# Optimization experiments

Measured on AMD Instinct MI355X. Metric: run time of the kernel, lower is better.

Reference implementation:

```python
import jax, jax.numpy as jnp
import numpy as np
from jax import lax

B, L, D_IN, H, RES, BD, D_OUT = 1024, 128, 5, 64, 256, 8, 1


def setup_inputs() -> dict:
    key = jax.random.key(0)
    ks = jax.random.split(key, 14)
    f = jnp.float32
    d = {}
    d["V_noise"] = jax.random.normal(ks[0], (B, D_IN), f)
    d["increments"] = jax.random.normal(ks[1], (B, L, BD), f)
    d["W1"] = jax.random.normal(ks[2], (H, D_IN), f) / np.float32(np.sqrt(D_IN))
    d["b1"] = jnp.zeros((H,), f)
    d["W2"] = jax.random.normal(ks[3], (RES, H), f) / np.float32(np.sqrt(H))
    d["b2"] = jnp.zeros((RES,), f)
    d["rho1"] = jax.random.normal(ks[4], (1, 1), f)
    d["rho2"] = jax.random.normal(ks[5], (1, 1), f)
    d["rho3"] = jax.random.normal(ks[6], (1, 1), f)
    d["rho4"] = jax.random.normal(ks[7], (1, 1), f)
    d["rho5"] = jax.random.normal(ks[8], (1, 1), f)
    # scale reservoir matrices by 1/sqrt(res) so pre-activations are O(1)
    d["B1"] = jax.random.normal(ks[9], (RES, RES), f) / np.float32(np.sqrt(RES))
    d["B2"] = jax.random.normal(ks[10], (BD, RES, RES), f) / np.float32(np.sqrt(RES))
    d["lambda1"] = jax.random.normal(ks[11], (RES, 1), f)
    d["lambda2"] = jax.random.normal(ks[12], (BD, RES, 1), f)
    d["Wr"] = jax.random.normal(ks[13], (D_OUT, RES), f) / np.float32(np.sqrt(RES))
    d["br"] = jnp.zeros((D_OUT,), f)
    return d


def reference(V_noise, increments, W1, b1, W2, b2,
              rho1, rho2, rho3, rho4, rho5,
              B1, B2, lambda1, lambda2, Wr, br):
    act = jnp.tanh
    # initial-condition MLP: [B, D_in] -> [B, RES]
    V = act(V_noise @ W1.T + b1) @ W2.T + b2
    # Brownian path with W[:,0] = 0
    Wp = jnp.cumsum(increments, axis=1).at[:, 0, :].set(0.0)
    dW = Wp[:, 1:] - Wp[:, :-1]          # [B, L-1, BD]
    l1 = lambda1[:, 0]                    # [RES]
    l2 = lambda2[:, :, 0]                 # [BD, RES]
    rho5s = rho5[0, 0]

    def step(r, dw):                      # r: [B, RES], dw: [B, BD]
        drift = act(rho1 * (r @ B1.T) + rho2 * l1)                      # [B, RES]
        diff = act(rho3 * jnp.einsum('kij,bj->bki', B2, r) + rho4 * l2)  # [B, BD, RES]
        rn = r + drift + rho5s * jnp.einsum('bki,bk->bi', diff, dw)
        return rn, rn

    _, Rs = lax.scan(step, V, jnp.swapaxes(dW, 0, 1))  # [L-1, B, RES]
    Rall = jnp.concatenate([V[None], Rs], axis=0)       # [L, B, RES]
    # time-homogeneous linear readout per lag, concatenated along time
    x = Rall @ Wr.T + br                                 # [L, B, D_out]
    out = jnp.transpose(x, (1, 0, 2)).reshape(V.shape[0], Rall.shape[0] * x.shape[-1], 1)
    return out
```

## Files before the change

### kernel.cpp

```cpp
#include <hip/hip_runtime.h>
#include <hip/hip_bf16.h>

#define B_TOT 1024
#define L_T   128
#define DIN   5
#define HD    64
#define RESN  256
#define BDN   8
#define NMAT  9
#define NROWS (NMAT * RESN)
#define PLANE ((size_t)NROWS * RESN)
#define NGRP  16
#define BG    64
#define FPB   16
#define NTHR  256
#define RB_GRP (2 * BG * RESN)
#define WS_RB_OFF  (2 * PLANE * 2)
#define WS_FLAG_OFF (WS_RB_OFF + (size_t)NGRP * RB_GRP * 4)
#define FLAGS_PER_GRP 1024

typedef __attribute__((ext_vector_type(8))) short bf16x8;
typedef __attribute__((ext_vector_type(4))) float f32x4;

__device__ __forceinline__ float fast_tanh(float x) {
    float e = __expf(2.0f * x);
    return 1.0f - 2.0f * __builtin_amdgcn_rcpf(e + 1.0f);
}

__device__ __forceinline__ unsigned pack_hilo(float v) {
    __hip_bfloat16 hi = __float2bfloat16(v);
    __hip_bfloat16 lo = __float2bfloat16(v - __bfloat162float(hi));
    return (unsigned)__builtin_bit_cast(unsigned short, hi) |
           ((unsigned)__builtin_bit_cast(unsigned short, lo) << 16);
}

__device__ __forceinline__ uint4 mall_load4(const unsigned* p) {
    uint4 r;
    asm volatile("global_load_dwordx4 %0, %1, off sc0 sc1" : "=v"(r) : "v"(p));
    return r;
}
__device__ __forceinline__ unsigned mall_load1(const unsigned* p) {
    unsigned r;
    asm volatile("global_load_dword %0, %1, off sc0 sc1" : "=v"(r) : "v"(p));
    return r;
}
__device__ __forceinline__ void mall_store1(unsigned* p, unsigned v) {
    asm volatile("global_store_dword %0, %1, off sc0 sc1" :: "v"(p), "v"(v) : "memory");
}
__device__ __forceinline__ void wait_vm0() {
    asm volatile("s_waitcnt vmcnt(0)" ::: "memory");
}

__device__ __forceinline__ void spin_all(const unsigned* fladdr, unsigned want) {
    unsigned guard = 0;
    for (;;) {
        unsigned fv = mall_load1(fladdr);
        wait_vm0();
        if (__ballot(fv < want) == 0ull) break;
        __builtin_amdgcn_s_sleep(1);
        if (++guard > (1u << 20)) break;
    }
}

__global__ void conv_w(const float* __restrict__ B1, const float* __restrict__ B2,
                       __hip_bfloat16* __restrict__ wh, __hip_bfloat16* __restrict__ wl) {
    int idx = blockIdx.x * 256 + threadIdx.x;
    float v = (idx < RESN * RESN) ? B1[idx] : B2[idx - RESN * RESN];
    __hip_bfloat16 h = __float2bfloat16(v);
    wh[idx] = h;
    wl[idx] = __float2bfloat16(v - __bfloat162float(h));
}

__global__ __launch_bounds__(NTHR, 1) void sde_ws(
    const float* __restrict__ Vn,  const float* __restrict__ inc,
    const float* __restrict__ W1,  const float* __restrict__ b1,
    const float* __restrict__ W2,  const float* __restrict__ b2,
    const float* __restrict__ rho1p, const float* __restrict__ rho2p,
    const float* __restrict__ rho3p, const float* __restrict__ rho4p,
    const float* __restrict__ rho5p,
    const float* __restrict__ lam1, const float* __restrict__ lam2,
    const float* __restrict__ Wr,  const float* __restrict__ brp,
    const __hip_bfloat16* __restrict__ wbf,
    unsigned int* __restrict__ rbu,
    unsigned int* __restrict__ flags,
    float* __restrict__ out)
{
    __shared__ __align__(16) short wlds[2][NMAT][8][64][8];
    __shared__ __align__(16) short wrlds[2][8][4][8];
    __shared__ __align__(16) short zfrag[8];

    const int tid  = threadIdx.x;
    const int mt   = tid >> 6;
    const int lane = tid & 63;
    const int n16  = lane & 15;
    const int quad = lane >> 4;
    const int bx   = blockIdx.x;
    const int g    = ((bx & 7) << 1) | (bx >> 7);
    const int fb   = (bx >> 3) & 15;
    const int f0   = fb * FPB;
    const int b0g  = g * BG;
    unsigned int* rbg    = rbu + (size_t)g * RB_GRP;
    unsigned int* flagp  = flags + g * FLAGS_PER_GRP;
    unsigned int* myflag = flagp + (fb * 4 + mt) * 16;
    const unsigned* fladdr = (const unsigned*)(flagp + ((lane & 15) * 4 + mt) * 16);

    const float rho1 = rho1p[0], rho2 = rho2p[0], rho3 = rho3p[0],
                rho4 = rho4p[0], rho5 = rho5p[0];
    const float brv = brp[0];

    float* hf  = (float*)&wlds[0][0][0][0][0];
    float* vsh = hf + 64 * 66;
    for (int p = tid; p < BG * HD; p += NTHR) {
        int b = p >> 6, hh = p & 63;
        float s = b1[hh];
        #pragma unroll
        for (int d = 0; d < DIN; ++d) s += Vn[(b0g + b) * DIN + d] * W1[hh * DIN + d];
        hf[b * 66 + hh] = fast_tanh(s);
    }
    __syncthreads();
    {
        int b = 16 * mt + (lane >> 2);
        #pragma unroll
        for (int i = 0; i < 4; ++i) {
            int f = (lane & 3) * 4 + i;
            float s = b2[f0 + f];
            #pragma unroll 8
            for (int hh = 0; hh < HD; ++hh) s += hf[b * 66 + hh] * W2[(f0 + f) * HD + hh];
            vsh[b * 16 + f] = s;
            mall_store1(&rbg[(0 * BG + b) * RESN + f0 + f], pack_hilo(s));
        }
    }
    wait_vm0();
    if (lane == 0)
        __hip_atomic_fetch_add(myflag, 1u, __ATOMIC_RELAXED, __HIP_MEMORY_SCOPE_AGENT);

    float rmast[4];
    #pragma unroll
    for (int rg = 0; rg < 4; ++rg) rmast[rg] = vsh[(16 * mt + 4 * quad + rg) * 16 + n16];
    const float l1c = lam1[f0 + n16];
    float l2c[BDN];
    #pragma unroll
    for (int k = 0; k < BDN; ++k) l2c[k] = lam2[k * RESN + f0 + n16];
    __syncthreads();

    for (int e = tid; e < 2 * NMAT * 8 * 64; e += NTHR) {
        int l  = e & 63;
        int kk = (e >> 6) & 7;
        int m  = e >> 9;
        int pl = (m >= NMAT) ? 1 : 0;
        int nt = m - pl * NMAT;
        const uint4* src = (const uint4*)(wbf + (size_t)pl * PLANE +
            (size_t)(nt * RESN + f0 + (l & 15)) * RESN + kk * 32 + (l >> 4) * 8);
        *(uint4*)&wlds[pl][nt][kk][l][0] = *src;
    }
    for (int p = tid; p < 512; p += NTHR) {
        int s = p >> 3, j = p & 7;
        int pl = s >> 5, kk = (s >> 2) & 7, q = s & 3;
        float v = Wr[kk * 32 + q * 8 + j];
        __hip_bfloat16 hi = __float2bfloat16(v);
        wrlds[pl][kk][q][j] = pl ? __builtin_bit_cast(short, __float2bfloat16(v - __bfloat162float(hi)))
                                 : __builtin_bit_cast(short, hi);
    }
    if (tid < 8) zfrag[tid] = 0;
    __syncthreads();

    const short* ph = (n16 == 0) ? &wrlds[0][0][quad][0] : &zfrag[0];
    const short* pw = (n16 == 0) ? &wrlds[1][0][quad][0] : &zfrag[0];
    const int    stp = (n16 == 0) ? 4 * 8 : 0;

    for (int t = 0; t < L_T - 1; ++t) {
        float dwv[4][8];
        #pragma unroll
        for (int rg = 0; rg < 4; ++rg) {
            const size_t bglob = (size_t)(b0g + 16 * mt + 4 * quad + rg) * (L_T * BDN);
            const float4 d0 = *(const float4*)(inc + bglob + (size_t)(t + 1) * BDN);
            const float4 d1 = *(const float4*)(inc + bglob + (size_t)(t + 1) * BDN + 4);
            dwv[rg][0] = d0.x; dwv[rg][1] = d0.y; dwv[rg][2] = d0.z; dwv[rg][3] = d0.w;
            dwv[rg][4] = d1.x; dwv[rg][5] = d1.y; dwv[rg][6] = d1.z; dwv[rg][7] = d1.w;
            if (t == 0) {
                const float4 e0 = *(const float4*)(inc + bglob);
                const float4 e1 = *(const float4*)(inc + bglob + 4);
                dwv[rg][0] += e0.x; dwv[rg][1] += e0.y; dwv[rg][2] += e0.z; dwv[rg][3] += e0.w;
                dwv[rg][4] += e1.x; dwv[rg][5] += e1.y; dwv[rg][6] += e1.z; dwv[rg][7] += e1.w;
            }
        }
        spin_all(fladdr, (unsigned)(t + 1));
        const int cur = t & 1, nxt = cur ^ 1;
        const int lead = t & 15;

        uint4 ua[16];
        {
            const unsigned* rbc = rbg + (size_t)(cur * BG + 16 * mt + n16) * RESN + quad * 8;
            #pragma unroll
            for (int kk = 0; kk < 8; ++kk) {
                ua[2 * kk]     = mall_load4(rbc + kk * 32);
                ua[2 * kk + 1] = mall_load4(rbc + kk * 32 + 4);
            }
        }
        wait_vm0();
        bf16x8 afh[8], afl[8];
        #pragma unroll
        for (int kk = 0; kk < 8; ++kk) {
            const uint4 a = ua[2 * kk], b = ua[2 * kk + 1];
            unsigned hw[4], lw[4];
            hw[0] = __builtin_amdgcn_perm(a.y, a.x, 0x05040100u);
            hw[1] = __builtin_amdgcn_perm(a.w, a.z, 0x05040100u);
            hw[2] = __builtin_amdgcn_perm(b.y, b.x, 0x05040100u);
            hw[3] = __builtin_amdgcn_perm(b.w, b.z, 0x05040100u);
            lw[0] = __builtin_amdgcn_perm(a.y, a.x, 0x07060302u);
            lw[1] = __builtin_amdgcn_perm(a.w, a.z, 0x07060302u);
            lw[2] = __builtin_amdgcn_perm(b.y, b.x, 0x07060302u);
            lw[3] = __builtin_amdgcn_perm(b.w, b.z, 0x07060302u);
            afh[kk] = __builtin_bit_cast(bf16x8, *(__attribute__((ext_vector_type(4))) unsigned*)hw);
            afl[kk] = __builtin_bit_cast(bf16x8, *(__attribute__((ext_vector_type(4))) unsigned*)lw);
        }

        f32x4 acc[NMAT] = {};
        #pragma unroll
        for (int kk = 0; kk < 8; ++kk) {
            bf16x8 bh[NMAT], bl[NMAT];
            #pragma unroll
            for (int nt = 0; nt < NMAT; ++nt) {
                bh[nt] = *(const bf16x8*)&wlds[0][nt][kk][lane][0];
                bl[nt] = *(const bf16x8*)&wlds[1][nt][kk][lane][0];
            }
            #pragma unroll
            for (int nt = 0; nt < NMAT; ++nt)
                acc[nt] = __builtin_amdgcn_mfma_f32_16x16x32_bf16(afh[kk], bh[nt], acc[nt], 0, 0, 0);
            #pragma unroll
            for (int nt = 0; nt < NMAT; ++nt)
                acc[nt] = __builtin_amdgcn_mfma_f32_16x16x32_bf16(afl[kk], bh[nt], acc[nt], 0, 0, 0);
            #pragma unroll
            for (int nt = 0; nt < NMAT; ++nt)
                acc[nt] = __builtin_amdgcn_mfma_f32_16x16x32_bf16(afh[kk], bl[nt], acc[nt], 0, 0, 0);
        }

        #pragma unroll
        for (int rg = 0; rg < 4; ++rg) {
            const int bl_ = 16 * mt + 4 * quad + rg;
            float drift = fast_tanh(rho1 * acc[0][rg] + rho2 * l1c);
            float s = 0.0f;
            #pragma unroll
            for (int k = 0; k < BDN; ++k)
                s += fast_tanh(rho3 * acc[1 + k][rg] + rho4 * l2c[k]) * dwv[rg][k];
            float rn = rmast[rg] + drift + rho5 * s;
            rmast[rg] = rn;
            mall_store1(&rbg[(nxt * BG + bl_) * RESN + f0 + n16], pack_hilo(rn));
        }
        wait_vm0();
        if (lane == 0)
            __hip_atomic_fetch_add(myflag, 1u, __ATOMIC_RELAXED, __HIP_MEMORY_SCOPE_AGENT);

        if (fb == lead) {
            f32x4 accw = {};
            #pragma unroll
            for (int kk = 0; kk < 8; ++kk) {
                bf16x8 wh8 = *(const bf16x8*)(ph + kk * stp);
                bf16x8 wl8 = *(const bf16x8*)(pw + kk * stp);
                accw = __builtin_amdgcn_mfma_f32_16x16x32_bf16(afh[kk], wh8, accw, 0, 0, 0);
                accw = __builtin_amdgcn_mfma_f32_16x16x32_bf16(afl[kk], wh8, accw, 0, 0, 0);
                accw = __builtin_amdgcn_mfma_f32_16x16x32_bf16(afh[kk], wl8, accw, 0, 0, 0);
            }
            if (n16 == 0) {
                #pragma unroll
                for (int rg = 0; rg < 4; ++rg)
                    out[(size_t)(b0g + 16 * mt + 4 * quad + rg) * L_T + t] = accw[rg] + brv;
            }
        }
    }

    if (fb == 15) {
        spin_all(fladdr, (unsigned)L_T);
        uint4 ua[16];
        const unsigned* rbc = rbg + (size_t)(1 * BG + 16 * mt + n16) * RESN + quad * 8;
        #pragma unroll
        for (int kk = 0; kk < 8; ++kk) {
            ua[2 * kk]     = mall_load4(rbc + kk * 32);
            ua[2 * kk + 1] = mall_load4(rbc + kk * 32 + 4);
        }
        wait_vm0();
        f32x4 accw = {};
        #pragma unroll
        for (int kk = 0; kk < 8; ++kk) {
            const uint4 a = ua[2 * kk], b = ua[2 * kk + 1];
            unsigned hw[4], lw[4];
            hw[0] = __builtin_amdgcn_perm(a.y, a.x, 0x05040100u);
            hw[1] = __builtin_amdgcn_perm(a.w, a.z, 0x05040100u);
            hw[2] = __builtin_amdgcn_perm(b.y, b.x, 0x05040100u);
            hw[3] = __builtin_amdgcn_perm(b.w, b.z, 0x05040100u);
            lw[0] = __builtin_amdgcn_perm(a.y, a.x, 0x07060302u);
            lw[1] = __builtin_amdgcn_perm(a.w, a.z, 0x07060302u);
            lw[2] = __builtin_amdgcn_perm(b.y, b.x, 0x07060302u);
            lw[3] = __builtin_amdgcn_perm(b.w, b.z, 0x07060302u);
            bf16x8 ah = __builtin_bit_cast(bf16x8, *(__attribute__((ext_vector_type(4))) unsigned*)hw);
            bf16x8 al = __builtin_bit_cast(bf16x8, *(__attribute__((ext_vector_type(4))) unsigned*)lw);
            bf16x8 wh8 = *(const bf16x8*)(ph + kk * stp);
            bf16x8 wl8 = *(const bf16x8*)(pw + kk * stp);
            accw = __builtin_amdgcn_mfma_f32_16x16x32_bf16(ah, wh8, accw, 0, 0, 0);
            accw = __builtin_amdgcn_mfma_f32_16x16x32_bf16(al, wh8, accw, 0, 0, 0);
            accw = __builtin_amdgcn_mfma_f32_16x16x32_bf16(ah, wl8, accw, 0, 0, 0);
        }
        if (n16 == 0) {
            #pragma unroll
            for (int rg = 0; rg < 4; ++rg)
                out[(size_t)(b0g + 16 * mt + 4 * quad + rg) * L_T + (L_T - 1)] = accw[rg] + brv;
        }
    }
}

extern "C" void kernel_launch(void* const* d_in, const int* in_sizes, int n_in,
                              void* d_out, int out_size, void* d_ws, size_t ws_size,
                              hipStream_t stream) {
    const float* Vn   = (const float*)d_in[0];
    const float* inc  = (const float*)d_in[1];
    const float* W1   = (const float*)d_in[2];
    const float* b1   = (const float*)d_in[3];
    const float* W2   = (const float*)d_in[4];
    const float* b2   = (const float*)d_in[5];
    const float* r1   = (const float*)d_in[6];
    const float* r2   = (const float*)d_in[7];
    const float* r3   = (const float*)d_in[8];
    const float* r4   = (const float*)d_in[9];
    const float* r5   = (const float*)d_in[10];
    const float* B1   = (const float*)d_in[11];
    const float* B2   = (const float*)d_in[12];
    const float* lam1 = (const float*)d_in[13];
    const float* lam2 = (const float*)d_in[14];
    const float* Wr   = (const float*)d_in[15];
    const float* br   = (const float*)d_in[16];

    __hip_bfloat16* wh    = (__hip_bfloat16*)d_ws;
    unsigned int*   rbu   = (unsigned int*)((char*)d_ws + WS_RB_OFF);
    unsigned int*   flags = (unsigned int*)((char*)d_ws + WS_FLAG_OFF);
    float* out = (float*)d_out;

    hipMemsetAsync(flags, 0, NGRP * FLAGS_PER_GRP * sizeof(unsigned int), stream);
    conv_w<<<dim3(NROWS * RESN / 256), dim3(256), 0, stream>>>(B1, B2, wh, wh + PLANE);
    sde_ws<<<dim3(256), dim3(NTHR), 0, stream>>>(
        Vn, inc, W1, b1, W2, b2, r1, r2, r3, r4, r5, lam1, lam2, Wr, br,
        wh, rbu, flags, out);
}
```

Measured before the change: 873.1 us.

## Replace flag-based inter-block sync with tagged data words and register-resident weights

The separate flag counters and atomic increments are removed. Each step now embeds a 2-bit step tag in the low bits of the packed hi/lo state words, and consumers spin directly on the state data until every tag matches. This drops one round trip of flag polling plus the store-drain wait per step. It also keeps 3 of the 9 weight matrices in registers and only 6 in LDS, and fuses the readout MFMA into the main k-loop. In exchange, the low bf16 word loses two mantissa bits, which slightly lowers precision, and register pressure rises.

```diff
diff --git a/kernel.cpp b/kernel.cpp
--- a/kernel.cpp
+++ b/kernel.cpp
@@ -8,6 +8,8 @@
 #define RESN  256
 #define BDN   8
 #define NMAT  9
+#define NMAT_REG 3
+#define NMAT_LDS 6
 #define NROWS (NMAT * RESN)
 #define PLANE ((size_t)NROWS * RESN)
 #define NGRP  16
@@ -16,8 +18,6 @@
 #define NTHR  256
 #define RB_GRP (2 * BG * RESN)
 #define WS_RB_OFF  (2 * PLANE * 2)
-#define WS_FLAG_OFF (WS_RB_OFF + (size_t)NGRP * RB_GRP * 4)
-#define FLAGS_PER_GRP 1024
 
 typedef __attribute__((ext_vector_type(8))) short bf16x8;
 typedef __attribute__((ext_vector_type(4))) float f32x4;
@@ -27,11 +27,12 @@
     return 1.0f - 2.0f * __builtin_amdgcn_rcpf(e + 1.0f);
 }
 
-__device__ __forceinline__ unsigned pack_hilo(float v) {
+__device__ __forceinline__ unsigned pack_hilo_tag(float v, unsigned tag16) {
     __hip_bfloat16 hi = __float2bfloat16(v);
     __hip_bfloat16 lo = __float2bfloat16(v - __bfloat162float(hi));
-    return (unsigned)__builtin_bit_cast(unsigned short, hi) |
-           ((unsigned)__builtin_bit_cast(unsigned short, lo) << 16);
+    unsigned pv = (unsigned)__builtin_bit_cast(unsigned short, hi) |
+                  ((unsigned)__builtin_bit_cast(unsigned short, lo) << 16);
+    return (pv & 0xFFFCFFFFu) | tag16;
 }
 
 __device__ __forceinline__ uint4 mall_load4(const unsigned* p) {
@@ -39,11 +40,6 @@
     asm volatile("global_load_dwordx4 %0, %1, off sc0 sc1" : "=v"(r) : "v"(p));
     return r;
 }
-__device__ __forceinline__ unsigned mall_load1(const unsigned* p) {
-    unsigned r;
-    asm volatile("global_load_dword %0, %1, off sc0 sc1" : "=v"(r) : "v"(p));
-    return r;
-}
 __device__ __forceinline__ void mall_store1(unsigned* p, unsigned v) {
     asm volatile("global_store_dword %0, %1, off sc0 sc1" :: "v"(p), "v"(v) : "memory");
 }
@@ -51,15 +47,19 @@
     asm volatile("s_waitcnt vmcnt(0)" ::: "memory");
 }
 
-__device__ __forceinline__ void spin_all(const unsigned* fladdr, unsigned want) {
-    unsigned guard = 0;
-    for (;;) {
-        unsigned fv = mall_load1(fladdr);
-        wait_vm0();
-        if (__ballot(fv < want) == 0ull) break;
-        __builtin_amdgcn_s_sleep(1);
-        if (++guard > (1u << 20)) break;
-    }
+__device__ __forceinline__ void unpack_af(const uint4 a, const uint4 b,
+                                          bf16x8& afh, bf16x8& afl) {
+    unsigned hw[4], lw[4];
+    hw[0] = __builtin_amdgcn_perm(a.y, a.x, 0x05040100u);
+    hw[1] = __builtin_amdgcn_perm(a.w, a.z, 0x05040100u);
+    hw[2] = __builtin_amdgcn_perm(b.y, b.x, 0x05040100u);
+    hw[3] = __builtin_amdgcn_perm(b.w, b.z, 0x05040100u);
+    lw[0] = __builtin_amdgcn_perm(a.y, a.x, 0x07060302u) & 0xFFFCFFFCu;
+    lw[1] = __builtin_amdgcn_perm(a.w, a.z, 0x07060302u) & 0xFFFCFFFCu;
+    lw[2] = __builtin_amdgcn_perm(b.y, b.x, 0x07060302u) & 0xFFFCFFFCu;
+    lw[3] = __builtin_amdgcn_perm(b.w, b.z, 0x07060302u) & 0xFFFCFFFCu;
+    afh = __builtin_bit_cast(bf16x8, *(__attribute__((ext_vector_type(4))) unsigned*)hw);
+    afl = __builtin_bit_cast(bf16x8, *(__attribute__((ext_vector_type(4))) unsigned*)lw);
 }
 
 __global__ void conv_w(const float* __restrict__ B1, const float* __restrict__ B2,
@@ -69,6 +69,12 @@
     __hip_bfloat16 h = __float2bfloat16(v);
     wh[idx] = h;
     wl[idx] = __float2bfloat16(v - __bfloat162float(h));
+}
+
+__global__ void init_rb(unsigned* __restrict__ rbu) {
+    unsigned idx = blockIdx.x * 256 + threadIdx.x;
+    unsigned buf = (idx & (RB_GRP - 1)) >> 14;
+    rbu[idx] = buf ? 0x00000000u : 0x00010000u;
 }
 
 __global__ __launch_bounds__(NTHR, 1) void sde_ws(
@@ -82,10 +88,9 @@
     const float* __restrict__ Wr,  const float* __restrict__ brp,
     const __hip_bfloat16* __restrict__ wbf,
     unsigned int* __restrict__ rbu,
-    unsigned int* __restrict__ flags,
     float* __restrict__ out)
 {
-    __shared__ __align__(16) short wlds[2][NMAT][8][64][8];
+    __shared__ __align__(16) short wlds[2][NMAT_LDS][8][64][8];
     __shared__ __align__(16) short wrlds[2][8][4][8];
     __shared__ __align__(16) short zfrag[8];
 
@@ -99,10 +104,7 @@
     const int fb   = (bx >> 3) & 15;
     const int f0   = fb * FPB;
     const int b0g  = g * BG;
-    unsigned int* rbg    = rbu + (size_t)g * RB_GRP;
-    unsigned int* flagp  = flags + g * FLAGS_PER_GRP;
-    unsigned int* myflag = flagp + (fb * 4 + mt) * 16;
-    const unsigned* fladdr = (const unsigned*)(flagp + ((lane & 15) * 4 + mt) * 16);
+    unsigned int* rbg = rbu + (size_t)g * RB_GRP;
 
     const float rho1 = rho1p[0], rho2 = rho2p[0], rho3 = rho3p[0],
                 rho4 = rho4p[0], rho5 = rho5p[0];
@@ -127,13 +129,9 @@
             #pragma unroll 8
             for (int hh = 0; hh < HD; ++hh) s += hf[b * 66 + hh] * W2[(f0 + f) * HD + hh];
             vsh[b * 16 + f] = s;
-            mall_store1(&rbg[(0 * BG + b) * RESN + f0 + f], pack_hilo(s));
-        }
-    }
-    wait_vm0();
-    if (lane == 0)
-        __hip_atomic_fetch_add(myflag, 1u, __ATOMIC_RELAXED, __HIP_MEMORY_SCOPE_AGENT);
-
+            mall_store1(&rbg[(0 * BG + b) * RESN + f0 + f], pack_hilo_tag(s, 0u));
+        }
+    }
     float rmast[4];
     #pragma unroll
     for (int rg = 0; rg < 4; ++rg) rmast[rg] = vsh[(16 * mt + 4 * quad + rg) * 16 + n16];
@@ -143,14 +141,23 @@
     for (int k = 0; k < BDN; ++k) l2c[k] = lam2[k * RESN + f0 + n16];
     __syncthreads();
 
-    for (int e = tid; e < 2 * NMAT * 8 * 64; e += NTHR) {
+    bf16x8 Brh[NMAT_REG][8], Brl[NMAT_REG][8];
+    #pragma unroll
+    for (int nt = 0; nt < NMAT_REG; ++nt)
+        #pragma unroll
+        for (int kk = 0; kk < 8; ++kk) {
+            const size_t a = (size_t)(nt * RESN + f0 + n16) * RESN + kk * 32 + quad * 8;
+            Brh[nt][kk] = *(const bf16x8*)(wbf + a);
+            Brl[nt][kk] = *(const bf16x8*)(wbf + PLANE + a);
+        }
+    for (int e = tid; e < 2 * NMAT_LDS * 8 * 64; e += NTHR) {
         int l  = e & 63;
         int kk = (e >> 6) & 7;
         int m  = e >> 9;
-        int pl = (m >= NMAT) ? 1 : 0;
-        int nt = m - pl * NMAT;
+        int pl = (m >= NMAT_LDS) ? 1 : 0;
+        int nt = m - pl * NMAT_LDS;
         const uint4* src = (const uint4*)(wbf + (size_t)pl * PLANE +
-            (size_t)(nt * RESN + f0 + (l & 15)) * RESN + kk * 32 + (l >> 4) * 8);
+            (size_t)((NMAT_REG + nt) * RESN + f0 + (l & 15)) * RESN + kk * 32 + (l >> 4) * 8);
         *(uint4*)&wlds[pl][nt][kk][l][0] = *src;
     }
     for (int p = tid; p < 512; p += NTHR) {
@@ -184,57 +191,66 @@
                 dwv[rg][4] += e1.x; dwv[rg][5] += e1.y; dwv[rg][6] += e1.z; dwv[rg][7] += e1.w;
             }
         }
-        spin_all(fladdr, (unsigned)(t + 1));
         const int cur = t & 1, nxt = cur ^ 1;
         const int lead = t & 15;
+        const unsigned exp16 = ((unsigned)(t & 3)) << 16;
+        const unsigned* rbc = rbg + (size_t)(cur * BG + 16 * mt + n16) * RESN + quad * 8;
 
         uint4 ua[16];
         {
-            const unsigned* rbc = rbg + (size_t)(cur * BG + 16 * mt + n16) * RESN + quad * 8;
-            #pragma unroll
-            for (int kk = 0; kk < 8; ++kk) {
-                ua[2 * kk]     = mall_load4(rbc + kk * 32);
-                ua[2 * kk + 1] = mall_load4(rbc + kk * 32 + 4);
-            }
-        }
-        wait_vm0();
-        bf16x8 afh[8], afl[8];
+            unsigned guard = 0;
+            for (;;) {
+                #pragma unroll
+                for (int kk = 0; kk < 8; ++kk) {
+                    ua[2 * kk]     = mall_load4(rbc + kk * 32);
+                    ua[2 * kk + 1] = mall_load4(rbc + kk * 32 + 4);
+                }
+                wait_vm0();
+                unsigned bad = 0;
+                #pragma unroll
+                for (int i = 0; i < 16; ++i)
+                    bad |= (ua[i].x ^ exp16) | (ua[i].y ^ exp16) |
+                           (ua[i].z ^ exp16) | (ua[i].w ^ exp16);
+                bad &= 0x00030000u;
+                if (__ballot(bad != 0) == 0ull) break;
+                __builtin_amdgcn_s_sleep(1);
+                if (++guard > (1u << 20)) break;
+            }
+        }
+
+        f32x4 acc[NMAT] = {};
+        f32x4 accw = {};
         #pragma unroll
         for (int kk = 0; kk < 8; ++kk) {
-            const uint4 a = ua[2 * kk], b = ua[2 * kk + 1];
-            unsigned hw[4], lw[4];
-            hw[0] = __builtin_amdgcn_perm(a.y, a.x, 0x05040100u);
-            hw[1] = __builtin_amdgcn_perm(a.w, a.z, 0x05040100u);
-            hw[2] = __builtin_amdgcn_perm(b.y, b.x, 0x05040100u);
-            hw[3] = __builtin_amdgcn_perm(b.w, b.z, 0x05040100u);
-            lw[0] = __builtin_amdgcn_perm(a.y, a.x, 0x07060302u);
-            lw[1] = __builtin_amdgcn_perm(a.w, a.z, 0x07060302u);
-            lw[2] = __builtin_amdgcn_perm(b.y, b.x, 0x07060302u);
-            lw[3] = __builtin_amdgcn_perm(b.w, b.z, 0x07060302u);
-            afh[kk] = __builtin_bit_cast(bf16x8, *(__attribute__((ext_vector_type(4))) unsigned*)hw);
-            afl[kk] = __builtin_bit_cast(bf16x8, *(__attribute__((ext_vector_type(4))) unsigned*)lw);
-        }
-
-        f32x4 acc[NMAT] = {};
-        #pragma unroll
-        for (int kk = 0; kk < 8; ++kk) {
+            bf16x8 afh, afl;
+            unpack_af(ua[2 * kk], ua[2 * kk + 1], afh, afl);
             bf16x8 bh[NMAT], bl[NMAT];
             #pragma unroll
-            for (int nt = 0; nt < NMAT; ++nt) {
-                bh[nt] = *(const bf16x8*)&wlds[0][nt][kk][lane][0];
-                bl[nt] = *(const bf16x8*)&wlds[1][nt][kk][lane][0];
+            for (int nt = 0; nt < NMAT_REG; ++nt) { bh[nt] = Brh[nt][kk]; bl[nt] = Brl[nt][kk]; }
+            #pragma unroll
+            for (int nt = 0; nt < NMAT_LDS; ++nt) {
+                bh[NMAT_REG + nt] = *(const bf16x8*)&wlds[0][nt][kk][lane][0];
+                bl[NMAT_REG + nt] = *(const bf16x8*)&wlds[1][nt][kk][lane][0];
             }
             #pragma unroll
             for (int nt = 0; nt < NMAT; ++nt)
-                acc[nt] = __builtin_amdgcn_mfma_f32_16x16x32_bf16(afh[kk], bh[nt], acc[nt], 0, 0, 0);
+                acc[nt] = __builtin_amdgcn_mfma_f32_16x16x32_bf16(afh, bh[nt], acc[nt], 0, 0, 0);
             #pragma unroll
             for (int nt = 0; nt < NMAT; ++nt)
-                acc[nt] = __builtin_amdgcn_mfma_f32_16x16x32_bf16(afl[kk], bh[nt], acc[nt], 0, 0, 0);
+                acc[nt] = __builtin_amdgcn_mfma_f32_16x16x32_bf16(afl, bh[nt], acc[nt], 0, 0, 0);
             #pragma unroll
             for (int nt = 0; nt < NMAT; ++nt)
-                acc[nt] = __builtin_amdgcn_mfma_f32_16x16x32_bf16(afh[kk], bl[nt], acc[nt], 0, 0, 0);
-        }
-
+                acc[nt] = __builtin_amdgcn_mfma_f32_16x16x32_bf16(afh, bl[nt], acc[nt], 0, 0, 0);
+            if (fb == lead) {
+                bf16x8 wh8 = *(const bf16x8*)(ph + kk * stp);
+                bf16x8 wl8 = *(const bf16x8*)(pw + kk * stp);
+                accw = __builtin_amdgcn_mfma_f32_16x16x32_bf16(afh, wh8, accw, 0, 0, 0);
+                accw = __builtin_amdgcn_mfma_f32_16x16x32_bf16(afl, wh8, accw, 0, 0, 0);
+                accw = __builtin_amdgcn_mfma_f32_16x16x32_bf16(afh, wl8, accw, 0, 0, 0);
+            }
+        }
+
+        const unsigned tag16 = ((unsigned)((t + 1) & 3)) << 16;
         #pragma unroll
         for (int rg = 0; rg < 4; ++rg) {
             const int bl_ = 16 * mt + 4 * quad + rg;
@@ -245,60 +261,48 @@
                 s += fast_tanh(rho3 * acc[1 + k][rg] + rho4 * l2c[k]) * dwv[rg][k];
             float rn = rmast[rg] + drift + rho5 * s;
             rmast[rg] = rn;
-            mall_store1(&rbg[(nxt * BG + bl_) * RESN + f0 + n16], pack_hilo(rn));
-        }
-        wait_vm0();
-        if (lane == 0)
-            __hip_atomic_fetch_add(myflag, 1u, __ATOMIC_RELAXED, __HIP_MEMORY_SCOPE_AGENT);
-
-        if (fb == lead) {
-            f32x4 accw = {};
+            mall_store1(&rbg[(nxt * BG + bl_) * RESN + f0 + n16], pack_hilo_tag(rn, tag16));
+        }
+
+        if (fb == lead && n16 == 0) {
+            #pragma unroll
+            for (int rg = 0; rg < 4; ++rg)
+                out[(size_t)(b0g + 16 * mt + 4 * quad + rg) * L_T + t] = accw[rg] + brv;
+        }
+    }
+
+    if (fb == 15) {
+        const unsigned exp16 = 3u << 16;
+        const unsigned* rbc = rbg + (size_t)(1 * BG + 16 * mt + n16) * RESN + quad * 8;
+        uint4 ua[16];
+        unsigned guard = 0;
+        for (;;) {
             #pragma unroll
             for (int kk = 0; kk < 8; ++kk) {
-                bf16x8 wh8 = *(const bf16x8*)(ph + kk * stp);
-                bf16x8 wl8 = *(const bf16x8*)(pw + kk * stp);
-                accw = __builtin_amdgcn_mfma_f32_16x16x32_bf16(afh[kk], wh8, accw, 0, 0, 0);
-                accw = __builtin_amdgcn_mfma_f32_16x16x32_bf16(afl[kk], wh8, accw, 0, 0, 0);
-                accw = __builtin_amdgcn_mfma_f32_16x16x32_bf16(afh[kk], wl8, accw, 0, 0, 0);
-            }
-            if (n16 == 0) {
-                #pragma unroll
-                for (int rg = 0; rg < 4; ++rg)
-                    out[(size_t)(b0g + 16 * mt + 4 * quad + rg) * L_T + t] = accw[rg] + brv;
-            }
-        }
-    }
-
-    if (fb == 15) {
-        spin_all(fladdr, (unsigned)L_T);
-        uint4 ua[16];
-        const unsigned* rbc = rbg + (size_t)(1 * BG + 16 * mt + n16) * RESN + quad * 8;
+                ua[2 * kk]     = mall_load4(rbc + kk * 32);
+                ua[2 * kk + 1] = mall_load4(rbc + kk * 32 + 4);
+            }
+            wait_vm0();
+            unsigned bad = 0;
+            #pragma unroll
+            for (int i = 0; i < 16; ++i)
+                bad |= (ua[i].x ^ exp16) | (ua[i].y ^ exp16) |
+                       (ua[i].z ^ exp16) | (ua[i].w ^ exp16);
+            bad &= 0x00030000u;
+            if (__ballot(bad != 0) == 0ull) break;
+            __builtin_amdgcn_s_sleep(1);
+            if (++guard > (1u << 20)) break;
+        }
+        f32x4 accw = {};
         #pragma unroll
         for (int kk = 0; kk < 8; ++kk) {
-            ua[2 * kk]     = mall_load4(rbc + kk * 32);
-            ua[2 * kk + 1] = mall_load4(rbc + kk * 32 + 4);
-        }
-        wait_vm0();
-        f32x4 accw = {};
-        #pragma unroll
-        for (int kk = 0; kk < 8; ++kk) {
-            const uint4 a = ua[2 * kk], b = ua[2 * kk + 1];
-            unsigned hw[4], lw[4];
-            hw[0] = __builtin_amdgcn_perm(a.y, a.x, 0x05040100u);
-            hw[1] = __builtin_amdgcn_perm(a.w, a.z, 0x05040100u);
-            hw[2] = __builtin_amdgcn_perm(b.y, b.x, 0x05040100u);
-            hw[3] = __builtin_amdgcn_perm(b.w, b.z, 0x05040100u);
-            lw[0] = __builtin_amdgcn_perm(a.y, a.x, 0x07060302u);
-            lw[1] = __builtin_amdgcn_perm(a.w, a.z, 0x07060302u);
-            lw[2] = __builtin_amdgcn_perm(b.y, b.x, 0x07060302u);
-            lw[3] = __builtin_amdgcn_perm(b.w, b.z, 0x07060302u);
-            bf16x8 ah = __builtin_bit_cast(bf16x8, *(__attribute__((ext_vector_type(4))) unsigned*)hw);
-            bf16x8 al = __builtin_bit_cast(bf16x8, *(__attribute__((ext_vector_type(4))) unsigned*)lw);
+            bf16x8 afh, afl;
+            unpack_af(ua[2 * kk], ua[2 * kk + 1], afh, afl);
             bf16x8 wh8 = *(const bf16x8*)(ph + kk * stp);
             bf16x8 wl8 = *(const bf16x8*)(pw + kk * stp);
-            accw = __builtin_amdgcn_mfma_f32_16x16x32_bf16(ah, wh8, accw, 0, 0, 0);
-            accw = __builtin_amdgcn_mfma_f32_16x16x32_bf16(al, wh8, accw, 0, 0, 0);
-            accw = __builtin_amdgcn_mfma_f32_16x16x32_bf16(ah, wl8, accw, 0, 0, 0);
+            accw = __builtin_amdgcn_mfma_f32_16x16x32_bf16(afh, wh8, accw, 0, 0, 0);
+            accw = __builtin_amdgcn_mfma_f32_16x16x32_bf16(afl, wh8, accw, 0, 0, 0);
+            accw = __builtin_amdgcn_mfma_f32_16x16x32_bf16(afh, wl8, accw, 0, 0, 0);
         }
         if (n16 == 0) {
             #pragma unroll
@@ -329,14 +333,13 @@
     const float* Wr   = (const float*)d_in[15];
     const float* br   = (const float*)d_in[16];
 
-    __hip_bfloat16* wh    = (__hip_bfloat16*)d_ws;
-    unsigned int*   rbu   = (unsigned int*)((char*)d_ws + WS_RB_OFF);
-    unsigned int*   flags = (unsigned int*)((char*)d_ws + WS_FLAG_OFF);
+    __hip_bfloat16* wh  = (__hip_bfloat16*)d_ws;
+    unsigned int*   rbu = (unsigned int*)((char*)d_ws + WS_RB_OFF);
     float* out = (float*)d_out;
 
-    hipMemsetAsync(flags, 0, NGRP * FLAGS_PER_GRP * sizeof(unsigned int), stream);
+    init_rb<<<dim3(NGRP * RB_GRP / 256), dim3(256), 0, stream>>>(rbu);
     conv_w<<<dim3(NROWS * RESN / 256), dim3(256), 0, stream>>>(B1, B2, wh, wh + PLANE);
     sde_ws<<<dim3(256), dim3(NTHR), 0, stream>>>(
         Vn, inc, W1, b1, W2, b2, r1, r2, r3, r4, r5, lam1, lam2, Wr, br,
-        wh, rbu, flags, out);
-}
+        wh, rbu, out);
+}
```

Measured after the change: 963.3 us. +10.3%, slower.

## Tag state values with step parity bits to skip flag spin; cache B matrices in registers

Applied to the files above, without the earlier changes.

Embeds a 2-bit step tag in the low bits of the low bf16 half of each stored state value. Readers load the state optimistically and only fall back to the flag spin-wait and a reload when any tag mismatches, which removes the flag round-trip from the common path. It also keeps the first three weight matrices' MFMA fragments in registers instead of reloading them from LDS every step. The tag costs a little precision in the low residual, and the added register pressure may cause spills; correctness relies on per-dword visibility of the tagged stores.

```diff
diff --git a/kernel.cpp b/kernel.cpp
--- a/kernel.cpp
+++ b/kernel.cpp
@@ -8,6 +8,7 @@
 #define RESN  256
 #define BDN   8
 #define NMAT  9
+#define NMAT_REG 3
 #define NROWS (NMAT * RESN)
 #define PLANE ((size_t)NROWS * RESN)
 #define NGRP  16
@@ -27,11 +28,12 @@
     return 1.0f - 2.0f * __builtin_amdgcn_rcpf(e + 1.0f);
 }
 
-__device__ __forceinline__ unsigned pack_hilo(float v) {
+__device__ __forceinline__ unsigned pack_hilo_tag(float v, unsigned tag16) {
     __hip_bfloat16 hi = __float2bfloat16(v);
     __hip_bfloat16 lo = __float2bfloat16(v - __bfloat162float(hi));
-    return (unsigned)__builtin_bit_cast(unsigned short, hi) |
-           ((unsigned)__builtin_bit_cast(unsigned short, lo) << 16);
+    unsigned pv = (unsigned)__builtin_bit_cast(unsigned short, hi) |
+                  ((unsigned)__builtin_bit_cast(unsigned short, lo) << 16);
+    return (pv & 0xFFFCFFFFu) | tag16;
 }
 
 __device__ __forceinline__ uint4 mall_load4(const unsigned* p) {
@@ -60,6 +62,21 @@
         __builtin_amdgcn_s_sleep(1);
         if (++guard > (1u << 20)) break;
     }
+}
+
+__device__ __forceinline__ void unpack_af(const uint4 a, const uint4 b,
+                                          bf16x8& afh, bf16x8& afl) {
+    unsigned hw[4], lw[4];
+    hw[0] = __builtin_amdgcn_perm(a.y, a.x, 0x05040100u);
+    hw[1] = __builtin_amdgcn_perm(a.w, a.z, 0x05040100u);
+    hw[2] = __builtin_amdgcn_perm(b.y, b.x, 0x05040100u);
+    hw[3] = __builtin_amdgcn_perm(b.w, b.z, 0x05040100u);
+    lw[0] = __builtin_amdgcn_perm(a.y, a.x, 0x07060302u) & 0xFFFCFFFCu;
+    lw[1] = __builtin_amdgcn_perm(a.w, a.z, 0x07060302u) & 0xFFFCFFFCu;
+    lw[2] = __builtin_amdgcn_perm(b.y, b.x, 0x07060302u) & 0xFFFCFFFCu;
+    lw[3] = __builtin_amdgcn_perm(b.w, b.z, 0x07060302u) & 0xFFFCFFFCu;
+    afh = __builtin_bit_cast(bf16x8, *(__attribute__((ext_vector_type(4))) unsigned*)hw);
+    afl = __builtin_bit_cast(bf16x8, *(__attribute__((ext_vector_type(4))) unsigned*)lw);
 }
 
 __global__ void conv_w(const float* __restrict__ B1, const float* __restrict__ B2,
@@ -127,7 +144,7 @@
             #pragma unroll 8
             for (int hh = 0; hh < HD; ++hh) s += hf[b * 66 + hh] * W2[(f0 + f) * HD + hh];
             vsh[b * 16 + f] = s;
-            mall_store1(&rbg[(0 * BG + b) * RESN + f0 + f], pack_hilo(s));
+            mall_store1(&rbg[(0 * BG + b) * RESN + f0 + f], pack_hilo_tag(s, 0u));
         }
     }
     wait_vm0();
@@ -163,6 +180,15 @@
     }
     if (tid < 8) zfrag[tid] = 0;
     __syncthreads();
+
+    bf16x8 Brh[NMAT_REG][8], Brl[NMAT_REG][8];
+    #pragma unroll
+    for (int nt = 0; nt < NMAT_REG; ++nt)
+        #pragma unroll
+        for (int kk = 0; kk < 8; ++kk) {
+            Brh[nt][kk] = *(const bf16x8*)&wlds[0][nt][kk][lane][0];
+            Brl[nt][kk] = *(const bf16x8*)&wlds[1][nt][kk][lane][0];
+        }
 
     const short* ph = (n16 == 0) ? &wrlds[0][0][quad][0] : &zfrag[0];
     const short* pw = (n16 == 0) ? &wrlds[1][0][quad][0] : &zfrag[0];
@@ -184,43 +210,48 @@
                 dwv[rg][4] += e1.x; dwv[rg][5] += e1.y; dwv[rg][6] += e1.z; dwv[rg][7] += e1.w;
             }
         }
-        spin_all(fladdr, (unsigned)(t + 1));
         const int cur = t & 1, nxt = cur ^ 1;
         const int lead = t & 15;
+        const unsigned exp16 = ((unsigned)(t & 3)) << 16;
+        const unsigned* rbc = rbg + (size_t)(cur * BG + 16 * mt + n16) * RESN + quad * 8;
 
         uint4 ua[16];
+        #pragma unroll
+        for (int kk = 0; kk < 8; ++kk) {
+            ua[2 * kk]     = mall_load4(rbc + kk * 32);
+            ua[2 * kk + 1] = mall_load4(rbc + kk * 32 + 4);
+        }
+        wait_vm0();
         {
-            const unsigned* rbc = rbg + (size_t)(cur * BG + 16 * mt + n16) * RESN + quad * 8;
-            #pragma unroll
-            for (int kk = 0; kk < 8; ++kk) {
-                ua[2 * kk]     = mall_load4(rbc + kk * 32);
-                ua[2 * kk + 1] = mall_load4(rbc + kk * 32 + 4);
-            }
-        }
-        wait_vm0();
+            unsigned bad = 0;
+            #pragma unroll
+            for (int i = 0; i < 16; ++i)
+                bad |= (ua[i].x ^ exp16) | (ua[i].y ^ exp16) |
+                       (ua[i].z ^ exp16) | (ua[i].w ^ exp16);
+            bad &= 0x00030000u;
+            if (__ballot(bad != 0) != 0ull) {
+                spin_all(fladdr, (unsigned)(t + 1));
+                #pragma unroll
+                for (int kk = 0; kk < 8; ++kk) {
+                    ua[2 * kk]     = mall_load4(rbc + kk * 32);
+                    ua[2 * kk + 1] = mall_load4(rbc + kk * 32 + 4);
+                }
+                wait_vm0();
+            }
+        }
         bf16x8 afh[8], afl[8];
         #pragma unroll
-        for (int kk = 0; kk < 8; ++kk) {
-            const uint4 a = ua[2 * kk], b = ua[2 * kk + 1];
-            unsigned hw[4], lw[4];
-            hw[0] = __builtin_amdgcn_perm(a.y, a.x, 0x05040100u);
-            hw[1] = __builtin_amdgcn_perm(a.w, a.z, 0x05040100u);
-            hw[2] = __builtin_amdgcn_perm(b.y, b.x, 0x05040100u);
-            hw[3] = __builtin_amdgcn_perm(b.w, b.z, 0x05040100u);
-            lw[0] = __builtin_amdgcn_perm(a.y, a.x, 0x07060302u);
-            lw[1] = __builtin_amdgcn_perm(a.w, a.z, 0x07060302u);
-            lw[2] = __builtin_amdgcn_perm(b.y, b.x, 0x07060302u);
-            lw[3] = __builtin_amdgcn_perm(b.w, b.z, 0x07060302u);
-            afh[kk] = __builtin_bit_cast(bf16x8, *(__attribute__((ext_vector_type(4))) unsigned*)hw);
-            afl[kk] = __builtin_bit_cast(bf16x8, *(__attribute__((ext_vector_type(4))) unsigned*)lw);
-        }
+        for (int kk = 0; kk < 8; ++kk)
+            unpack_af(ua[2 * kk], ua[2 * kk + 1], afh[kk], afl[kk]);
 
         f32x4 acc[NMAT] = {};
         #pragma unroll
         for (int kk = 0; kk < 8; ++kk) {
             bf16x8 bh[NMAT], bl[NMAT];
             #pragma unroll
-            for (int nt = 0; nt < NMAT; ++nt) {
+            for (int nt = 0; nt < NMAT_REG; ++nt) { bh[nt] = Brh[nt][kk]; bl[nt] = Brl[nt][kk]; }
+            #pragma unroll
+            for (int nt = NMAT_REG; nt < NMAT; ++nt) {
                 bh[nt] = *(const bf16x8*)&wlds[0][nt][kk][lane][0];
                 bl[nt] = *(const bf16x8*)&wlds[1][nt][kk][lane][0];
             }
@@ -235,6 +266,7 @@
                 acc[nt] = __builtin_amdgcn_mfma_f32_16x16x32_bf16(afh[kk], bl[nt], acc[nt], 0, 0, 0);
         }
 
+        const unsigned tag16 = ((unsigned)((t + 1) & 3)) << 16;
         #pragma unroll
         for (int rg = 0; rg < 4; ++rg) {
             const int bl_ = 16 * mt + 4 * quad + rg;
@@ -245,7 +277,7 @@
                 s += fast_tanh(rho3 * acc[1 + k][rg] + rho4 * l2c[k]) * dwv[rg][k];
             float rn = rmast[rg] + drift + rho5 * s;
             rmast[rg] = rn;
-            mall_store1(&rbg[(nxt * BG + bl_) * RESN + f0 + n16], pack_hilo(rn));
+            mall_store1(&rbg[(nxt * BG + bl_) * RESN + f0 + n16], pack_hilo_tag(rn, tag16));
         }
         wait_vm0();
         if (lane == 0)
@@ -282,18 +314,8 @@
         f32x4 accw = {};
         #pragma unroll
         for (int kk = 0; kk < 8; ++kk) {
-            const uint4 a = ua[2 * kk], b = ua[2 * kk + 1];
-            unsigned hw[4], lw[4];
-            hw[0] = __builtin_amdgcn_perm(a.y, a.x, 0x05040100u);
-            hw[1] = __builtin_amdgcn_perm(a.w, a.z, 0x05040100u);
-            hw[2] = __builtin_amdgcn_perm(b.y, b.x, 0x05040100u);
-            hw[3] = __builtin_amdgcn_perm(b.w, b.z, 0x05040100u);
-            lw[0] = __builtin_amdgcn_perm(a.y, a.x, 0x07060302u);
-            lw[1] = __builtin_amdgcn_perm(a.w, a.z, 0x07060302u);
-            lw[2] = __builtin_amdgcn_perm(b.y, b.x, 0x07060302u);
-            lw[3] = __builtin_amdgcn_perm(b.w, b.z, 0x07060302u);
-            bf16x8 ah = __builtin_bit_cast(bf16x8, *(__attribute__((ext_vector_type(4))) unsigned*)hw);
-            bf16x8 al = __builtin_bit_cast(bf16x8, *(__attribute__((ext_vector_type(4))) unsigned*)lw);
+            bf16x8 ah, al;
+            unpack_af(ua[2 * kk], ua[2 * kk + 1], ah, al);
             bf16x8 wh8 = *(const bf16x8*)(ph + kk * stp);
             bf16x8 wl8 = *(const bf16x8*)(pw + kk * stp);
             accw = __builtin_amdgcn_mfma_f32_16x16x32_bf16(ah, wh8, accw, 0, 0, 0);
```

New measurement: 1.359 ms. 55.6% more time.
